# Kernel optimization log

Hardware: AMD Instinct MI355X
Metric: run time of the kernel (lower is better)

Reference implementation:

```python
import jax, jax.numpy as jnp
import numpy as np

B, T, C, H, W = 16, 8, 2048, 16, 8
C8, C4, HW, NP = C // 8, C // 4, H * W, T // 2


def _cbr(x, w, s, b):
    # 1x1 conv + folded BN (eval-mode affine) + ReLU; x: (N, Cin, H, W), w: (Cout, Cin)
    y = jnp.einsum('oc,nchw->nohw', w, x)
    return jax.nn.relu(y * s[None, :, None, None] + b[None, :, None, None])


def setup_inputs():
    key = jax.random.key(0)
    ks = jax.random.split(key, 16)
    r = lambda i, shape, sc: jax.random.normal(ks[i], shape, jnp.float32) * sc
    return dict(
        featmap=r(0, (B, T, C, H, W), 1.0),
        re_featmap=r(1, (B * T, C, H, W), 1.0),
        vect_featmap=r(2, (B, T, C), 1.0),
        embed_feat=r(3, (B, T, 128, H, W), 1.0),
        gamma_w=r(4, (C8, C), 0.03), gamma_s=jnp.ones((C8,)), gamma_b=jnp.zeros((C8,)),
        beta_w=r(5, (C8, C), 0.03), beta_s=jnp.ones((C8,)), beta_b=jnp.zeros((C8,)),
        gg_w=r(6, (128, 2 * HW), 0.05), gg_s=jnp.ones((128,)), gg_b=jnp.zeros((128,)),
        tte_w=r(7, (128, 256), 0.05), tte_s=jnp.ones((128,)), tte_b=jnp.zeros((128,)),
        te_w=r(8, (1, 256), 0.05), te_s=jnp.ones((1,)), te_b=jnp.zeros((1,)),
        theta_w=r(9, (C8, C), 0.03), theta_b=jnp.zeros((C8,)),
        cp_w1=r(10, (C8, C4), 0.05), cp_b1=jnp.zeros((C8,)),
        cp_w2=r(11, (C, C8), 0.05), cp_b2=jnp.zeros((C,)),
    )


def reference(featmap, re_featmap, vect_featmap, embed_feat,
              gamma_w, gamma_s, gamma_b, beta_w, beta_s, beta_b,
              gg_w, gg_s, gg_b, tte_w, tte_s, tte_b, te_w, te_s, te_b,
              theta_w, theta_b, cp_w1, cp_b1, cp_w2, cp_b2):
    # spatial attention embeddings: (B, T, C8, HW)
    gamma = _cbr(re_featmap, gamma_w, gamma_s, gamma_b).reshape(B, T, C8, HW)
    beta = _cbr(re_featmap, beta_w, beta_s, beta_b).reshape(B, T, C8, HW)

    # channel attention: Conv1d over time of (B, C, T) -> (B, C8, T)
    cp = jax.nn.relu(jnp.einsum('oc,btc->bot', theta_w, vect_featmap) + theta_b[None, :, None])
    cp = cp.reshape(B, C8, NP, 2)
    c0 = cp[..., 0].transpose(0, 2, 1)  # (B, NP, C8)
    c1 = cp[..., 1].transpose(0, 2, 1)

    def mlp(x):  # (B, NP, C4) -> sigmoid gate (B, NP, C)
        h1 = jax.nn.relu(x @ cp_w1.T + cp_b1)
        return jax.nn.sigmoid(h1 @ cp_w2.T + cp_b2)

    p00 = mlp(jnp.concatenate([c0, c1], -1))  # (B, NP, C)
    p01 = mlp(jnp.concatenate([c1, c0], -1))

    # pairwise spatial graphs
    g0, g1 = gamma[:, 0::2], gamma[:, 1::2]  # (B, NP, C8, HW)
    b0, b1 = beta[:, 0::2], beta[:, 1::2]
    Gs0 = jnp.einsum('bpcs,bpct->bpst', g0, b1)  # (B, NP, HW, HW)
    Gs1 = jnp.einsum('bpcs,bpct->bpst', g1, b0)
    # Gs_in = Gs^T viewed as (HW, H, W); Gs_out = Gs viewed likewise
    j0 = jnp.concatenate([Gs0.transpose(0, 1, 3, 2), Gs1], 2).reshape(B * NP, 2 * HW, H, W)
    j1 = jnp.concatenate([Gs1.transpose(0, 1, 3, 2), Gs0], 2).reshape(B * NP, 2 * HW, H, W)
    gj0 = _cbr(j0, gg_w, gg_s, gg_b)  # (B*NP, 128, H, W)
    gj1 = _cbr(j1, gg_w, gg_s, gg_b)

    ef = embed_feat.reshape(B, NP, 2, 128, H, W)
    e0 = ef[:, :, 0].reshape(B * NP, 128, H, W)
    e1 = ef[:, :, 1].reshape(B * NP, 128, H, W)
    ta = _cbr(jnp.concatenate([e0, e1], 1), tte_w, tte_s, tte_b)  # (B*NP, 128, H, W)
    tb = _cbr(jnp.concatenate([e1, e0], 1), tte_w, tte_s, tte_b)

    def gate(t_feat, gj):  # conv 256->1 + BN + sigmoid
        y = jnp.einsum('oc,nchw->nohw', te_w, jnp.concatenate([t_feat, gj], 1))
        return jax.nn.sigmoid(y * te_s[None, :, None, None] + te_b[None, :, None, None])

    pa = gate(ta, gj0).reshape(B, NP, 1, H, W)
    pb = gate(tb, gj1).reshape(B, NP, 1, H, W)

    f = featmap.reshape(B, NP, 2, C, H, W)
    gate0 = p00[..., None, None] * pa  # (B, NP, C, H, W)
    gate1 = p01[..., None, None] * pb
    out = jax.nn.relu(gate0 * f[:, :, 0] + gate1 * f[:, :, 1])
    return out * out  # (B, T//2, C, H, W)
```

## Files before the change

kernel.cpp:

```cpp
#include <hip/hip_runtime.h>
#include <stdint.h>


typedef _Float16 f16;
typedef _Float16 f16x4 __attribute__((ext_vector_type(4)));
typedef _Float16 f16x8 __attribute__((ext_vector_type(8)));
typedef float f32x4 __attribute__((ext_vector_type(4)));

typedef const void __attribute__((address_space(1)))* gptr1;
typedef void __attribute__((address_space(3)))* lptr3;

__device__ __forceinline__ void gload16(const void* g, void* l) {
  __builtin_amdgcn_global_load_lds((gptr1)g, (lptr3)l, 16, 0, 0);
}

__device__ __forceinline__ float sigmoidf_(float x) { return 1.f / (1.f + expf(-x)); }

#define WAIT_VM6 asm volatile("s_waitcnt vmcnt(6)" ::: "memory")
#define WAIT_VM0 asm volatile("s_waitcnt vmcnt(0)" ::: "memory")
#define WAIT_LGKM8 asm volatile("s_waitcnt lgkmcnt(8)" ::: "memory")
#define WAIT_LGKM0 asm volatile("s_waitcnt lgkmcnt(0)" ::: "memory")

__global__ __launch_bounds__(256) void kPP(const float* __restrict__ x,
                                           f16* __restrict__ Af,
                                           const float* __restrict__ gw, const float* __restrict__ gs,
                                           const float* __restrict__ bw, const float* __restrict__ bs,
                                           const float* __restrict__ gg_w, const float* __restrict__ gg_s,
                                           const float* __restrict__ tte_w, const float* __restrict__ tte_s,
                                           const float* __restrict__ thw, const float* __restrict__ w1,
                                           const float* __restrict__ w2,
                                           f16* __restrict__ Wf,
                                           float* __restrict__ ggT, float* __restrict__ tteT,
                                           float* __restrict__ thwT, float* __restrict__ w1T,
                                           float* __restrict__ w2T) {
  __shared__ __align__(16) char shmem[64 * 65 * 4];
  int t = threadIdx.x;
  int bid = blockIdx.x;
  if (bid < 8192) {
    float (*L)[65] = (float(*)[65])shmem;
    int n = bid >> 6;
    int kc = (bid >> 1) & 31;
    int hh = bid & 1;
    int k0 = kc * 64;
    const float* src = x + (size_t)n * 262144 + (size_t)k0 * 128 + hh * 64;
    for (int r = 0; r < 4; ++r) {
      int f = r * 256 + t;
      int kk = f >> 4, c4 = (f & 15) * 4;
      float4 v = *(const float4*)(src + (size_t)kk * 128 + c4);
      L[kk][c4 + 0] = v.x; L[kk][c4 + 1] = v.y; L[kk][c4 + 2] = v.z; L[kk][c4 + 3] = v.w;
    }
    __syncthreads();
    for (int r = 0; r < 2; ++r) {
      int id = r * 256 + t;
      int hw = id >> 3, c = id & 7;
      int cs = c ^ (hw & 7);
      f16x8 h8;
      for (int j = 0; j < 8; ++j)
        h8[j] = (f16)L[cs * 8 + j][hw];
      size_t m = (size_t)n * 128 + hh * 64 + hw;
      size_t ob = m * 2048 + (size_t)k0 + (size_t)c * 8;
      *(f16x8*)(Af + ob) = h8;
    }
    return;
  }
  if (bid < 8704) {
    int id = (bid - 8192) * 256 + t;
    int o = id >> 8, cch = id & 255;
    float s; const float* row;
    if (o < 256) { s = gs[o]; row = gw + (size_t)o * 2048; }
    else         { s = bs[o - 256]; row = bw + (size_t)(o - 256) * 2048; }
    int kb = cch >> 3, sub = cch & 7;
    int subd = sub ^ (o & 7);
    f16x8 h8;
    for (int j = 0; j < 8; ++j)
      h8[j] = (f16)(row[cch * 8 + j] * s);
    size_t ob = (size_t)o * 2048 + (size_t)kb * 64 + (size_t)subd * 8;
    *(f16x8*)(Wf + ob) = h8;
    return;
  }
  float (*TL)[65] = (float(*)[65])shmem;
  int tb = bid - 8704;
  const float* src; float* dst; const float* scale = nullptr; int R, C;
  if (tb < 128)      { src = thw;   dst = thwT; R = 256;  C = 2048; }
  else if (tb < 256) { tb -= 128; src = w2;  dst = w2T;  R = 2048; C = 256; }
  else if (tb < 288) { tb -= 256; src = w1;  dst = w1T;  R = 256;  C = 512; }
  else if (tb < 296) { tb -= 288; src = gg_w;  dst = ggT;  scale = gg_s;  R = 128; C = 256; }
  else               { tb -= 296; src = tte_w; dst = tteT; scale = tte_s; R = 128; C = 256; }
  int tpc = C >> 6;
  int r0 = (tb / tpc) * 64, c0 = (tb % tpc) * 64;
  int i16 = t >> 4, j4 = (t & 15) * 4;
  for (int s = 0; s < 4; ++s) {
    int i = i16 + s * 16;
    float4 v = *(const float4*)(src + (size_t)(r0 + i) * C + c0 + j4);
    TL[i][j4 + 0] = v.x; TL[i][j4 + 1] = v.y; TL[i][j4 + 2] = v.z; TL[i][j4 + 3] = v.w;
  }
  __syncthreads();
  for (int s = 0; s < 4; ++s) {
    int j = i16 + s * 16;
    float4 w;
    w.x = TL[j4 + 0][j]; w.y = TL[j4 + 1][j]; w.z = TL[j4 + 2][j]; w.w = TL[j4 + 3][j];
    if (scale) {
      w.x *= scale[r0 + j4 + 0]; w.y *= scale[r0 + j4 + 1];
      w.z *= scale[r0 + j4 + 2]; w.w *= scale[r0 + j4 + 3];
    }
    *(float4*)(dst + (size_t)(c0 + j) * R + r0 + j4) = w;
  }
}

__global__ __launch_bounds__(512, 2) void kGemm8(const f16* __restrict__ Af, const f16* __restrict__ Wf,
                                                 const float* __restrict__ gamma_b, const float* __restrict__ beta_b,
                                                 f16* __restrict__ gammaFh, f16* __restrict__ betaFh) {
  __shared__ __align__(16) f16 S[3][24576];
  int t = threadIdx.x;
  int lane = t & 63, wid = t >> 6;
  int wr = wid >> 2, wc = wid & 3;
  int bid = blockIdx.x;
  int bx = (bid & 7) * 16 + (bid >> 4);
  int by = (bid >> 3) & 1;
  size_t M0 = (size_t)bx * 128;
  size_t N0 = (size_t)by * 256;
  int row8 = wid * 8 + (lane >> 3);
  int sl = lane & 7;
  int fr = lane & 15, fq = lane >> 4;
  f32x4 acc[4][4] = {};
  f16x8 a[8], b[8];

  const char* AB = (const char*)Af;
  const char* WB = (const char*)Wf;
  const size_t aoff0 = (M0 + row8) * 4096 + (size_t)sl * 16;
  const size_t aoff1 = (M0 + 64 + row8) * 4096 + (size_t)sl * 16;
  const size_t woff0 = (N0 + row8) * 4096 + (size_t)sl * 16;
  const size_t woff1 = (N0 + 64 + row8) * 4096 + (size_t)sl * 16;
  const size_t woff2 = (N0 + 128 + row8) * 4096 + (size_t)sl * 16;
  const size_t woff3 = (N0 + 192 + row8) * 4096 + (size_t)sl * 16;

#define STAGE_ALL(dst, s) do {                                                     \
    int koff_ = (s) << 7;                                                          \
    char* l_ = (char*)(dst) + wid * 1024;                                          \
    gload16(AB + aoff0 + koff_, l_);                                               \
    gload16(AB + aoff1 + koff_, l_ + 8192);                                        \
    gload16(WB + woff0 + koff_, l_ + 16384);                                       \
    gload16(WB + woff1 + koff_, l_ + 24576);                                       \
    gload16(WB + woff2 + koff_, l_ + 32768);                                       \
    gload16(WB + woff3 + koff_, l_ + 40960);                                       \
  } while (0)

#define LOADG(buf, g) do {                                                         \
    const f16* bA_ = (const f16*)(buf);                                            \
    const f16* bB_ = bA_ + 8192;                                                   \
    int cg_ = (g) * 4 + fq;                                                        \
    _Pragma("unroll") for (int mi = 0; mi < 4; ++mi) {                             \
      int m_ = wr * 64 + mi * 16 + fr;                                             \
      a[(g) * 4 + mi] = *(const f16x8*)(bA_ + m_ * 64 + ((cg_ ^ (m_ & 7)) << 3));  \
    }                                                                              \
    _Pragma("unroll") for (int ni = 0; ni < 4; ++ni) {                             \
      int n_ = wc * 64 + ni * 16 + fr;                                             \
      b[(g) * 4 + ni] = *(const f16x8*)(bB_ + n_ * 64 + ((cg_ ^ (n_ & 7)) << 3));  \
    }                                                                              \
  } while (0)

#define STEP(rdbuf, stbuf, kt) do {                                                \
    if ((kt) < 31) { WAIT_VM6; } else { WAIT_VM0; }                                \
    __builtin_amdgcn_s_barrier();                                                  \
    if ((kt) <= 29) STAGE_ALL(stbuf, (kt) + 2);                                    \
    LOADG(rdbuf, 0);                                                               \
    __builtin_amdgcn_sched_barrier(0);                                             \
    LOADG(rdbuf, 1);                                                               \
    WAIT_LGKM8;                                                                    \
    __builtin_amdgcn_sched_barrier(0);                                             \
    __builtin_amdgcn_s_setprio(1);                                                 \
    _Pragma("unroll") for (int mi = 0; mi < 4; ++mi)                               \
      _Pragma("unroll") for (int ni = 0; ni < 4; ++ni)                             \
        acc[mi][ni] = __builtin_amdgcn_mfma_f32_16x16x32_f16(a[mi], b[ni], acc[mi][ni], 0, 0, 0); \
    WAIT_LGKM0;                                                                    \
    __builtin_amdgcn_sched_barrier(0);                                             \
    _Pragma("unroll") for (int mi = 0; mi < 4; ++mi)                               \
      _Pragma("unroll") for (int ni = 0; ni < 4; ++ni)                             \
        acc[mi][ni] = __builtin_amdgcn_mfma_f32_16x16x32_f16(a[4 + mi], b[4 + ni], acc[mi][ni], 0, 0, 0); \
    __builtin_amdgcn_s_setprio(0);                                                 \
  } while (0)

  STAGE_ALL(&S[0][0], 0);
  STAGE_ALL(&S[1][0], 1);
  for (int base = 0; base < 30; base += 3) {
    STEP(&S[0][0], &S[2][0], base);
    STEP(&S[1][0], &S[0][0], base + 1);
    STEP(&S[2][0], &S[1][0], base + 2);
  }
  STEP(&S[0][0], &S[2][0], 30);
  STEP(&S[1][0], &S[0][0], 31);
#undef STEP
#undef LOADG
#undef STAGE_ALL

  const float* bias = by ? beta_b : gamma_b;
  f16* outb = by ? betaFh : gammaFh;
#pragma unroll
  for (int mi = 0; mi < 4; ++mi) {
    int hwb = wr * 64 + mi * 16 + fq * 4;
#pragma unroll
    for (int ni = 0; ni < 4; ++ni) {
      int o = wc * 64 + ni * 16 + fr;
      float bb = bias[o];
      f32x4 v = acc[mi][ni];
      f16x4 w;
      w[0] = (f16)fmaxf(v[0] + bb, 0.f);
      w[1] = (f16)fmaxf(v[1] + bb, 0.f);
      w[2] = (f16)fmaxf(v[2] + bb, 0.f);
      w[3] = (f16)fmaxf(v[3] + bb, 0.f);
      *(f16x4*)(outb + (size_t)bx * 32768 + (size_t)o * 128 + hwb) = w;
    }
  }
}

__global__ __launch_bounds__(256) void kTT(const float* __restrict__ vect, const float* __restrict__ thwT,
                                           float* __restrict__ P,
                                           const float* __restrict__ embed, const float* __restrict__ tteT,
                                           const float* __restrict__ tte_b, const float* __restrict__ te_w,
                                           float* __restrict__ Sta) {
  __shared__ float V[512];
  __shared__ __align__(16) float E[256 * 64];
  __shared__ float Red2[2][16 * 64];
  int bid = blockIdx.x;
  int t = threadIdx.x;
  if (bid < 512) {
    int bt = bid & 127, kq = bid >> 7;
    const float* src = vect + (size_t)bt * 2048 + kq * 512;
    if (t < 128) *(float4*)(V + t * 4) = *(const float4*)(src + t * 4);
    __syncthreads();
    const float* wp = thwT + (size_t)kq * 512 * 256 + t;
    float acc = 0.f;
#pragma unroll 8
    for (int c = 0; c < 512; ++c)
      acc = fmaf(wp[(size_t)c * 256], V[c], acc);
    P[((size_t)kq * 128 + bt) * 256 + t] = acc;
    return;
  }
  int i = bid - 512;
  int n = i & 63, hh = (i >> 6) & 1;
  int b = n >> 2, p = n & 3;
  const float* eA = embed + (size_t)(b * 8 + 2 * p) * 16384 + hh * 64;
  const float* eB = embed + (size_t)(b * 8 + 2 * p + 1) * 16384 + hh * 64;
  for (int r = 0; r < 8; ++r) {
    int f = r * 256 + t;
    int ch = f >> 4, q = (f & 15) * 4;
    *(float4*)(E + ch * 64 + q) = *(const float4*)(eA + (size_t)ch * 128 + q);
  }
  for (int r = 0; r < 8; ++r) {
    int f = r * 256 + t;
    int ch = f >> 4, q = (f & 15) * 4;
    *(float4*)(E + (128 + ch) * 64 + q) = *(const float4*)(eB + (size_t)ch * 128 + q);
  }
  __syncthreads();
  int ty = t >> 4, tx = t & 15;
  float acc0[8][4] = {}, acc1[8][4] = {};
  for (int c = 0; c < 256; ++c) {
    float w8a[8], w8b[8];
    *(float4*)w8a = *(const float4*)(tteT + (size_t)c * 128 + ty * 8);
    *(float4*)(w8a + 4) = *(const float4*)(tteT + (size_t)c * 128 + ty * 8 + 4);
    int c2 = c ^ 128;
    *(float4*)w8b = *(const float4*)(tteT + (size_t)c2 * 128 + ty * 8);
    *(float4*)(w8b + 4) = *(const float4*)(tteT + (size_t)c2 * 128 + ty * 8 + 4);
    float4 g = *(const float4*)(E + c * 64 + tx * 4);
    for (int ii = 0; ii < 8; ++ii) {
      acc0[ii][0] = fmaf(w8a[ii], g.x, acc0[ii][0]);
      acc0[ii][1] = fmaf(w8a[ii], g.y, acc0[ii][1]);
      acc0[ii][2] = fmaf(w8a[ii], g.z, acc0[ii][2]);
      acc0[ii][3] = fmaf(w8a[ii], g.w, acc0[ii][3]);
      acc1[ii][0] = fmaf(w8b[ii], g.x, acc1[ii][0]);
      acc1[ii][1] = fmaf(w8b[ii], g.y, acc1[ii][1]);
      acc1[ii][2] = fmaf(w8b[ii], g.z, acc1[ii][2]);
      acc1[ii][3] = fmaf(w8b[ii], g.w, acc1[ii][3]);
    }
  }
  float par0[4] = {0.f, 0.f, 0.f, 0.f};
  float par1[4] = {0.f, 0.f, 0.f, 0.f};
  for (int ii = 0; ii < 8; ++ii) {
    int o = ty * 8 + ii;
    float tb = tte_b[o], tw = te_w[o];
    for (int j = 0; j < 4; ++j) {
      par0[j] += tw * fmaxf(acc0[ii][j] + tb, 0.f);
      par1[j] += tw * fmaxf(acc1[ii][j] + tb, 0.f);
    }
  }
  for (int j = 0; j < 4; ++j) {
    Red2[0][ty * 64 + tx * 4 + j] = par0[j];
    Red2[1][ty * 64 + tx * 4 + j] = par1[j];
  }
  __syncthreads();
  if (t < 128) {
    int g = t >> 6, tt = t & 63;
    float s = 0.f;
    for (int q = 0; q < 16; ++q) s += Red2[g][q * 64 + tt];
    Sta[(size_t)g * 8192 + n * 128 + hh * 64 + tt] = s;
  }
}

__global__ __launch_bounds__(256) void kAG(const float* __restrict__ P, const float* __restrict__ thb,
                                           const float* __restrict__ w1T, const float* __restrict__ b1,
                                           float* __restrict__ h1,
                                           const f16* __restrict__ gammaFh, const f16* __restrict__ betaFh,
                                           float* __restrict__ Gs0, float* __restrict__ Gs1) {
  __shared__ float x0[256], x1[256];
  __shared__ float ra[256], rb[256];
  __shared__ __align__(16) float As[16 * 128];
  __shared__ __align__(16) float Bs[16 * 64];
  int bid = blockIdx.x;
  int t = threadIdx.x;
  if (bid < 256) {
    int bp = bid & 63, och = bid >> 6;
    int b = bp >> 2, p = bp & 3;
    int bt0 = b * 8 + 2 * p, bt1 = bt0 + 1;
    {
      float a0 = 0.f, a1 = 0.f;
      for (int q = 0; q < 4; ++q) {
        a0 += P[((size_t)q * 128 + bt0) * 256 + t];
        a1 += P[((size_t)q * 128 + bt1) * 256 + t];
      }
      float tb = thb[t];
      x0[t] = fmaxf(a0 + tb, 0.f);
      x1[t] = fmaxf(a1 + tb, 0.f);
    }
    __syncthreads();
    int o = och * 64 + (t & 63);
    int ks = t >> 6;
    const float* xa = (ks < 2) ? x0 : x1;
    const float* xb = (ks < 2) ? x1 : x0;
    int kbase = ks * 128;
    int xoff = (ks < 2) ? kbase : kbase - 256;
    float aa = 0.f, ab = 0.f;
#pragma unroll 8
    for (int ii = 0; ii < 128; ++ii) {
      float w = w1T[(size_t)(kbase + ii) * 256 + o];
      aa = fmaf(w, xa[xoff + ii], aa);
      ab = fmaf(w, xb[xoff + ii], ab);
    }
    ra[t] = aa;
    rb[t] = ab;
    __syncthreads();
    if (t < 64) {
      float sa = ra[t] + ra[64 + t] + ra[128 + t] + ra[192 + t];
      float sb = rb[t] + rb[64 + t] + rb[128 + t] + rb[192 + t];
      float bb = b1[o];
      h1[((size_t)bp * 2) * 256 + o] = fmaxf(sa + bb, 0.f);
      h1[((size_t)bp * 2 + 1) * 256 + o] = fmaxf(sb + bb, 0.f);
    }
    return;
  }
  int i = bid - 256;
  int n = i & 63, which = (i >> 6) & 1, th = (i >> 7) & 1;
  int b = n >> 2, p = n & 3;
  int tg = 2 * p + which;
  int tb = 2 * p + 1 - which;
  const f16* A = gammaFh + (size_t)(b * 8 + tg) * 32768;
  const f16* Bm = betaFh + (size_t)(b * 8 + tb) * 32768;
  float* out = (which ? Gs1 : Gs0) + (size_t)n * 16384;
  int ty = t >> 4, tx = t & 15;
  float acc[8][4] = {};
  for (int c0 = 0; c0 < 256; c0 += 16) {
    {
      int cc = t >> 4, col8 = (t & 15) * 8;
      f16x8 v = *(const f16x8*)(A + (size_t)(c0 + cc) * 128 + col8);
      for (int j = 0; j < 8; ++j) As[cc * 128 + col8 + j] = (float)v[j];
    }
    if (t < 128) {
      int cc = t >> 3, col8 = (t & 7) * 8;
      f16x8 v = *(const f16x8*)(Bm + (size_t)(c0 + cc) * 128 + th * 64 + col8);
      for (int j = 0; j < 8; ++j) Bs[cc * 64 + col8 + j] = (float)v[j];
    }
    __syncthreads();
    for (int cc = 0; cc < 16; ++cc) {
      float a8[8];
      *(float4*)a8 = *(const float4*)(As + cc * 128 + ty * 8);
      *(float4*)(a8 + 4) = *(const float4*)(As + cc * 128 + ty * 8 + 4);
      float4 b4 = *(const float4*)(Bs + cc * 64 + tx * 4);
      for (int ii = 0; ii < 8; ++ii) {
        acc[ii][0] = fmaf(a8[ii], b4.x, acc[ii][0]);
        acc[ii][1] = fmaf(a8[ii], b4.y, acc[ii][1]);
        acc[ii][2] = fmaf(a8[ii], b4.z, acc[ii][2]);
        acc[ii][3] = fmaf(a8[ii], b4.w, acc[ii][3]);
      }
    }
    __syncthreads();
  }
  for (int ii = 0; ii < 8; ++ii) {
    *(float4*)(out + (size_t)(ty * 8 + ii) * 128 + th * 64 + tx * 4) =
        make_float4(acc[ii][0], acc[ii][1], acc[ii][2], acc[ii][3]);
  }
}

__global__ __launch_bounds__(256) void kBG(const float* __restrict__ h1, const float* __restrict__ w2T,
                                           const float* __restrict__ b2,
                                           float* __restrict__ p00, float* __restrict__ p01,
                                           const float* __restrict__ Gs0, const float* __restrict__ Gs1,
                                           const float* __restrict__ ggT, const float* __restrict__ gg_b,
                                           const float* __restrict__ te_w, float* __restrict__ Sgj) {
  __shared__ float ha[256], hb[256];
  __shared__ float G0h[64 * 129];
  __shared__ __align__(16) float G1c[128 * 64];
  __shared__ float Red[16 * 64];
  int bid = blockIdx.x;
  int t = threadIdx.x;
  if (bid < 512) {
    int bp = bid & 63, chc = bid >> 6;
    ha[t] = h1[((size_t)bp * 2) * 256 + t];
    hb[t] = h1[((size_t)bp * 2 + 1) * 256 + t];
    __syncthreads();
    int ch = chc * 256 + t;
    float sa = 0.f, sb = 0.f;
#pragma unroll 8
    for (int k = 0; k < 256; ++k) {
      float w = w2T[(size_t)k * 2048 + ch];
      sa = fmaf(w, ha[k], sa);
      sb = fmaf(w, hb[k], sb);
    }
    p00[(size_t)bp * 2048 + ch] = sigmoidf_(sa + b2[ch]);
    p01[(size_t)bp * 2048 + ch] = sigmoidf_(sb + b2[ch]);
    return;
  }
  int i = bid - 512;
  int n = i & 63, gate = (i >> 6) & 1, hh = (i >> 7) & 1;
  const float* srcT = (gate == 0 ? Gs0 : Gs1) + (size_t)n * 16384;
  const float* srcC = (gate == 0 ? Gs1 : Gs0) + (size_t)n * 16384;
  for (int r = 0; r < 8; ++r) {
    int f = r * 256 + t;
    int hwl = f >> 5, c4 = (f & 31) * 4;
    float4 v = *(const float4*)(srcT + (size_t)(hh * 64 + hwl) * 128 + c4);
    G0h[hwl * 129 + c4 + 0] = v.x;
    G0h[hwl * 129 + c4 + 1] = v.y;
    G0h[hwl * 129 + c4 + 2] = v.z;
    G0h[hwl * 129 + c4 + 3] = v.w;
  }
  for (int r = 0; r < 8; ++r) {
    int f = r * 256 + t;
    int c = f >> 4, q = (f & 15) * 4;
    *(float4*)(G1c + c * 64 + q) = *(const float4*)(srcC + (size_t)c * 128 + hh * 64 + q);
  }
  __syncthreads();
  int ty = t >> 4, tx = t & 15;
  float acc[8][4] = {};
  for (int c = 0; c < 128; ++c) {
    float w8[8];
    *(float4*)w8 = *(const float4*)(ggT + (size_t)c * 128 + ty * 8);
    *(float4*)(w8 + 4) = *(const float4*)(ggT + (size_t)c * 128 + ty * 8 + 4);
    float g4[4];
    for (int j = 0; j < 4; ++j) g4[j] = G0h[(tx * 4 + j) * 129 + c];
    for (int ii = 0; ii < 8; ++ii)
      for (int j = 0; j < 4; ++j)
        acc[ii][j] = fmaf(w8[ii], g4[j], acc[ii][j]);
  }
  for (int c = 0; c < 128; ++c) {
    float w8[8];
    *(float4*)w8 = *(const float4*)(ggT + (size_t)(128 + c) * 128 + ty * 8);
    *(float4*)(w8 + 4) = *(const float4*)(ggT + (size_t)(128 + c) * 128 + ty * 8 + 4);
    float4 g = *(const float4*)(G1c + c * 64 + tx * 4);
    for (int ii = 0; ii < 8; ++ii) {
      acc[ii][0] = fmaf(w8[ii], g.x, acc[ii][0]);
      acc[ii][1] = fmaf(w8[ii], g.y, acc[ii][1]);
      acc[ii][2] = fmaf(w8[ii], g.z, acc[ii][2]);
      acc[ii][3] = fmaf(w8[ii], g.w, acc[ii][3]);
    }
  }
  float par[4] = {0.f, 0.f, 0.f, 0.f};
  for (int ii = 0; ii < 8; ++ii) {
    int o = ty * 8 + ii;
    float gb = gg_b[o], tw = te_w[128 + o];
    for (int j = 0; j < 4; ++j)
      par[j] += tw * fmaxf(acc[ii][j] + gb, 0.f);
  }
  for (int j = 0; j < 4; ++j) Red[ty * 64 + tx * 4 + j] = par[j];
  __syncthreads();
  if (t < 64) {
    float s = 0.f;
    for (int g = 0; g < 16; ++g) s += Red[g * 64 + t];
    Sgj[(size_t)gate * 8192 + n * 128 + hh * 64 + t] = s;
  }
}

__global__ __launch_bounds__(256) void kFinal(const float* __restrict__ featmap, const float* __restrict__ p00,
                                              const float* __restrict__ p01, const float* __restrict__ Sta,
                                              const float* __restrict__ Sgj, const float* __restrict__ te_s,
                                              const float* __restrict__ te_b, float* __restrict__ out) {
  int fid = blockIdx.x * 256 + threadIdx.x;
  int h4 = (fid & 31) * 4;
  int c = (fid >> 5) & 2047;
  int bp = fid >> 16;
  int b = bp >> 2, p = bp & 3;
  float ga = p00[(size_t)bp * 2048 + c];
  float gb = p01[(size_t)bp * 2048 + c];
  float ts = te_s[0], tbv = te_b[0];
  float4 sa0 = *(const float4*)(Sta + (size_t)bp * 128 + h4);
  float4 sg0 = *(const float4*)(Sgj + (size_t)bp * 128 + h4);
  float4 sa1 = *(const float4*)(Sta + 8192 + (size_t)bp * 128 + h4);
  float4 sg1 = *(const float4*)(Sgj + 8192 + (size_t)bp * 128 + h4);
  float4 pa4, pb4;
  pa4.x = sigmoidf_(ts * (sa0.x + sg0.x) + tbv);
  pa4.y = sigmoidf_(ts * (sa0.y + sg0.y) + tbv);
  pa4.z = sigmoidf_(ts * (sa0.z + sg0.z) + tbv);
  pa4.w = sigmoidf_(ts * (sa0.w + sg0.w) + tbv);
  pb4.x = sigmoidf_(ts * (sa1.x + sg1.x) + tbv);
  pb4.y = sigmoidf_(ts * (sa1.y + sg1.y) + tbv);
  pb4.z = sigmoidf_(ts * (sa1.z + sg1.z) + tbv);
  pb4.w = sigmoidf_(ts * (sa1.w + sg1.w) + tbv);
  const float* f0 = featmap + (size_t)(b * 8 + 2 * p) * 262144 + (size_t)c * 128 + h4;
  const float* f1 = f0 + 262144;
  float4 v0 = *(const float4*)f0;
  float4 v1 = *(const float4*)f1;
  float4 o4;
  float r;
  r = fmaxf(ga * pa4.x * v0.x + gb * pb4.x * v1.x, 0.f); o4.x = r * r;
  r = fmaxf(ga * pa4.y * v0.y + gb * pb4.y * v1.y, 0.f); o4.y = r * r;
  r = fmaxf(ga * pa4.z * v0.z + gb * pb4.z * v1.z, 0.f); o4.z = r * r;
  r = fmaxf(ga * pa4.w * v0.w + gb * pb4.w * v1.w, 0.f); o4.w = r * r;
  *(float4*)(out + (size_t)fid * 4) = o4;
}

extern "C" void kernel_launch(void* const* d_in, const int* in_sizes, int n_in,
                              void* d_out, int out_size, void* d_ws, size_t ws_size,
                              hipStream_t stream) {
  (void)in_sizes; (void)n_in; (void)out_size; (void)ws_size;
  const float* featmap    = (const float*)d_in[0];
  const float* re_featmap = (const float*)d_in[1];
  const float* vect       = (const float*)d_in[2];
  const float* embed      = (const float*)d_in[3];
  const float* gamma_w    = (const float*)d_in[4];
  const float* gamma_s    = (const float*)d_in[5];
  const float* gamma_b    = (const float*)d_in[6];
  const float* beta_w     = (const float*)d_in[7];
  const float* beta_s     = (const float*)d_in[8];
  const float* beta_b     = (const float*)d_in[9];
  const float* gg_w       = (const float*)d_in[10];
  const float* gg_s       = (const float*)d_in[11];
  const float* gg_b       = (const float*)d_in[12];
  const float* tte_w      = (const float*)d_in[13];
  const float* tte_s      = (const float*)d_in[14];
  const float* tte_b      = (const float*)d_in[15];
  const float* te_w       = (const float*)d_in[16];
  const float* te_s       = (const float*)d_in[17];
  const float* te_b       = (const float*)d_in[18];
  const float* theta_w    = (const float*)d_in[19];
  const float* theta_b    = (const float*)d_in[20];
  const float* cp_w1      = (const float*)d_in[21];
  const float* cp_b1      = (const float*)d_in[22];
  const float* cp_w2      = (const float*)d_in[23];
  const float* cp_b2      = (const float*)d_in[24];
  float* out = (float*)d_out;

  char* w = (char*)d_ws;
  f16* Af  = (f16*)w;   w += (size_t)16384 * 2048 * 2;
  f16* Wf  = (f16*)w;   w += (size_t)512 * 2048 * 2;
  f16* gammaFh = (f16*)w; w += (size_t)128 * 256 * 128 * 2;
  f16* betaFh  = (f16*)w; w += (size_t)128 * 256 * 128 * 2;
  float* Gs0    = (float*)w; w += (size_t)64 * 128 * 128 * 4;
  float* Gs1    = (float*)w; w += (size_t)64 * 128 * 128 * 4;
  float* ggT    = (float*)w; w += (size_t)256 * 128 * 4;
  float* tteT   = (float*)w; w += (size_t)256 * 128 * 4;
  float* thwT   = (float*)w; w += (size_t)2048 * 256 * 4;
  float* w1T    = (float*)w; w += (size_t)512 * 256 * 4;
  float* w2T    = (float*)w; w += (size_t)256 * 2048 * 4;
  float* P      = (float*)w; w += (size_t)4 * 128 * 256 * 4;
  float* h1     = (float*)w; w += (size_t)64 * 2 * 256 * 4;
  float* Sta    = (float*)w; w += (size_t)2 * 64 * 128 * 4;
  float* Sgj    = (float*)w; w += (size_t)2 * 64 * 128 * 4;
  float* p00    = (float*)w; w += (size_t)64 * 2048 * 4;
  float* p01    = (float*)w; w += (size_t)64 * 2048 * 4;

  kPP<<<9008, 256, 0, stream>>>(re_featmap, Af,
                                gamma_w, gamma_s, beta_w, beta_s, gg_w, gg_s, tte_w, tte_s,
                                theta_w, cp_w1, cp_w2, Wf, ggT, tteT, thwT, w1T, w2T);
  kGemm8<<<256, 512, 0, stream>>>(Af, Wf, gamma_b, beta_b, gammaFh, betaFh);
  kTT<<<640, 256, 0, stream>>>(vect, thwT, P, embed, tteT, tte_b, te_w, Sta);
  kAG<<<512, 256, 0, stream>>>(P, theta_b, w1T, cp_b1, h1, gammaFh, betaFh, Gs0, Gs1);
  kBG<<<768, 256, 0, stream>>>(h1, w2T, cp_b2, p00, p01, Gs0, Gs1, ggT, gg_b, te_w, Sgj);
  kFinal<<<16384, 256, 0, stream>>>(featmap, p00, p01, Sta, Sgj, te_s, te_b, out);
}
```

Baseline: 269.5 us.

## Merge mid-stage kernels into two launches and shrink shared memory

Merges the three middle kernels (kTT, kAG, kBG) into two. The gamma·beta GEMM moves into the first launch next to the theta projection and the tte embedding. The whole channel MLP (theta reduce, fc1, fc2, sigmoid) now runs in one block per batch-pair, so the h1 intermediate buffer is gone. The tte path is re-tiled to 32-column halves, which doubles its block count and cuts its shared memory. The gg path reads one operand straight from global memory instead of staging it in LDS. This removes one launch and a global round-trip and should raise occupancy through smaller LDS arenas. The cost is that the MLP now runs on only 64 serial-heavy blocks, each doing 512+2048-channel dot loops.

```diff
diff --git a/kernel.cpp b/kernel.cpp
--- a/kernel.cpp
+++ b/kernel.cpp
@@ -213,17 +213,18 @@
   }
 }
 
-__global__ __launch_bounds__(256) void kTT(const float* __restrict__ vect, const float* __restrict__ thwT,
+__global__ __launch_bounds__(256) void kM1(const float* __restrict__ vect, const float* __restrict__ thwT,
                                            float* __restrict__ P,
                                            const float* __restrict__ embed, const float* __restrict__ tteT,
                                            const float* __restrict__ tte_b, const float* __restrict__ te_w,
-                                           float* __restrict__ Sta) {
-  __shared__ float V[512];
-  __shared__ __align__(16) float E[256 * 64];
-  __shared__ float Red2[2][16 * 64];
+                                           float* __restrict__ Sta,
+                                           const f16* __restrict__ gammaFh, const f16* __restrict__ betaFh,
+                                           float* __restrict__ Gs0, float* __restrict__ Gs1) {
+  __shared__ __align__(16) char arena[36992];
   int bid = blockIdx.x;
   int t = threadIdx.x;
   if (bid < 512) {
+    float* V = (float*)arena;
     int bt = bid & 127, kq = bid >> 7;
     const float* src = vect + (size_t)bt * 2048 + kq * 512;
     if (t < 128) *(float4*)(V + t * 4) = *(const float4*)(src + t * 4);
@@ -236,118 +237,67 @@
     P[((size_t)kq * 128 + bt) * 256 + t] = acc;
     return;
   }
-  int i = bid - 512;
-  int n = i & 63, hh = (i >> 6) & 1;
-  int b = n >> 2, p = n & 3;
-  const float* eA = embed + (size_t)(b * 8 + 2 * p) * 16384 + hh * 64;
-  const float* eB = embed + (size_t)(b * 8 + 2 * p + 1) * 16384 + hh * 64;
-  for (int r = 0; r < 8; ++r) {
-    int f = r * 256 + t;
-    int ch = f >> 4, q = (f & 15) * 4;
-    *(float4*)(E + ch * 64 + q) = *(const float4*)(eA + (size_t)ch * 128 + q);
-  }
-  for (int r = 0; r < 8; ++r) {
-    int f = r * 256 + t;
-    int ch = f >> 4, q = (f & 15) * 4;
-    *(float4*)(E + (128 + ch) * 64 + q) = *(const float4*)(eB + (size_t)ch * 128 + q);
-  }
-  __syncthreads();
-  int ty = t >> 4, tx = t & 15;
-  float acc0[8][4] = {}, acc1[8][4] = {};
-  for (int c = 0; c < 256; ++c) {
-    float w8a[8], w8b[8];
-    *(float4*)w8a = *(const float4*)(tteT + (size_t)c * 128 + ty * 8);
-    *(float4*)(w8a + 4) = *(const float4*)(tteT + (size_t)c * 128 + ty * 8 + 4);
-    int c2 = c ^ 128;
-    *(float4*)w8b = *(const float4*)(tteT + (size_t)c2 * 128 + ty * 8);
-    *(float4*)(w8b + 4) = *(const float4*)(tteT + (size_t)c2 * 128 + ty * 8 + 4);
-    float4 g = *(const float4*)(E + c * 64 + tx * 4);
+  if (bid < 768) {
+    float* E = (float*)arena;
+    float* Red2 = (float*)(arena + 32768);
+    int i = bid - 512;
+    int n = i & 63, hq = i >> 6;
+    int b = n >> 2, p = n & 3;
+    const float* eA = embed + (size_t)(b * 8 + 2 * p) * 16384 + hq * 32;
+    const float* eB = eA + 16384;
+    for (int r = 0; r < 4; ++r) {
+      int f = r * 256 + t;
+      int ch = f >> 3, q = (f & 7) * 4;
+      *(float4*)(E + ch * 32 + q) = *(const float4*)(eA + (size_t)ch * 128 + q);
+    }
+    for (int r = 0; r < 4; ++r) {
+      int f = r * 256 + t;
+      int ch = f >> 3, q = (f & 7) * 4;
+      *(float4*)(E + (128 + ch) * 32 + q) = *(const float4*)(eB + (size_t)ch * 128 + q);
+    }
+    __syncthreads();
+    int ty = t >> 4, tx = t & 15;
+    float acc0[8][2] = {}, acc1[8][2] = {};
+    for (int c = 0; c < 256; ++c) {
+      float w8a[8], w8b[8];
+      *(float4*)w8a = *(const float4*)(tteT + (size_t)c * 128 + ty * 8);
+      *(float4*)(w8a + 4) = *(const float4*)(tteT + (size_t)c * 128 + ty * 8 + 4);
+      int c2 = c ^ 128;
+      *(float4*)w8b = *(const float4*)(tteT + (size_t)c2 * 128 + ty * 8);
+      *(float4*)(w8b + 4) = *(const float4*)(tteT + (size_t)c2 * 128 + ty * 8 + 4);
+      float2 g = *(const float2*)(E + c * 32 + tx * 2);
+      for (int ii = 0; ii < 8; ++ii) {
+        acc0[ii][0] = fmaf(w8a[ii], g.x, acc0[ii][0]);
+        acc0[ii][1] = fmaf(w8a[ii], g.y, acc0[ii][1]);
+        acc1[ii][0] = fmaf(w8b[ii], g.x, acc1[ii][0]);
+        acc1[ii][1] = fmaf(w8b[ii], g.y, acc1[ii][1]);
+      }
+    }
+    float par0[2] = {0.f, 0.f}, par1[2] = {0.f, 0.f};
     for (int ii = 0; ii < 8; ++ii) {
-      acc0[ii][0] = fmaf(w8a[ii], g.x, acc0[ii][0]);
-      acc0[ii][1] = fmaf(w8a[ii], g.y, acc0[ii][1]);
-      acc0[ii][2] = fmaf(w8a[ii], g.z, acc0[ii][2]);
-      acc0[ii][3] = fmaf(w8a[ii], g.w, acc0[ii][3]);
-      acc1[ii][0] = fmaf(w8b[ii], g.x, acc1[ii][0]);
-      acc1[ii][1] = fmaf(w8b[ii], g.y, acc1[ii][1]);
-      acc1[ii][2] = fmaf(w8b[ii], g.z, acc1[ii][2]);
-      acc1[ii][3] = fmaf(w8b[ii], g.w, acc1[ii][3]);
-    }
-  }
-  float par0[4] = {0.f, 0.f, 0.f, 0.f};
-  float par1[4] = {0.f, 0.f, 0.f, 0.f};
-  for (int ii = 0; ii < 8; ++ii) {
-    int o = ty * 8 + ii;
-    float tb = tte_b[o], tw = te_w[o];
-    for (int j = 0; j < 4; ++j) {
-      par0[j] += tw * fmaxf(acc0[ii][j] + tb, 0.f);
-      par1[j] += tw * fmaxf(acc1[ii][j] + tb, 0.f);
-    }
-  }
-  for (int j = 0; j < 4; ++j) {
-    Red2[0][ty * 64 + tx * 4 + j] = par0[j];
-    Red2[1][ty * 64 + tx * 4 + j] = par1[j];
-  }
-  __syncthreads();
-  if (t < 128) {
-    int g = t >> 6, tt = t & 63;
-    float s = 0.f;
-    for (int q = 0; q < 16; ++q) s += Red2[g][q * 64 + tt];
-    Sta[(size_t)g * 8192 + n * 128 + hh * 64 + tt] = s;
-  }
-}
-
-__global__ __launch_bounds__(256) void kAG(const float* __restrict__ P, const float* __restrict__ thb,
-                                           const float* __restrict__ w1T, const float* __restrict__ b1,
-                                           float* __restrict__ h1,
-                                           const f16* __restrict__ gammaFh, const f16* __restrict__ betaFh,
-                                           float* __restrict__ Gs0, float* __restrict__ Gs1) {
-  __shared__ float x0[256], x1[256];
-  __shared__ float ra[256], rb[256];
-  __shared__ __align__(16) float As[16 * 128];
-  __shared__ __align__(16) float Bs[16 * 64];
-  int bid = blockIdx.x;
-  int t = threadIdx.x;
-  if (bid < 256) {
-    int bp = bid & 63, och = bid >> 6;
-    int b = bp >> 2, p = bp & 3;
-    int bt0 = b * 8 + 2 * p, bt1 = bt0 + 1;
-    {
-      float a0 = 0.f, a1 = 0.f;
-      for (int q = 0; q < 4; ++q) {
-        a0 += P[((size_t)q * 128 + bt0) * 256 + t];
-        a1 += P[((size_t)q * 128 + bt1) * 256 + t];
+      int o = ty * 8 + ii;
+      float tb = tte_b[o], tw = te_w[o];
+      for (int j = 0; j < 2; ++j) {
+        par0[j] += tw * fmaxf(acc0[ii][j] + tb, 0.f);
+        par1[j] += tw * fmaxf(acc1[ii][j] + tb, 0.f);
       }
-      float tb = thb[t];
-      x0[t] = fmaxf(a0 + tb, 0.f);
-      x1[t] = fmaxf(a1 + tb, 0.f);
-    }
-    __syncthreads();
-    int o = och * 64 + (t & 63);
-    int ks = t >> 6;
-    const float* xa = (ks < 2) ? x0 : x1;
-    const float* xb = (ks < 2) ? x1 : x0;
-    int kbase = ks * 128;
-    int xoff = (ks < 2) ? kbase : kbase - 256;
-    float aa = 0.f, ab = 0.f;
-#pragma unroll 8
-    for (int ii = 0; ii < 128; ++ii) {
-      float w = w1T[(size_t)(kbase + ii) * 256 + o];
-      aa = fmaf(w, xa[xoff + ii], aa);
-      ab = fmaf(w, xb[xoff + ii], ab);
-    }
-    ra[t] = aa;
-    rb[t] = ab;
+    }
+    for (int j = 0; j < 2; ++j) {
+      Red2[0 * 512 + ty * 32 + tx * 2 + j] = par0[j];
+      Red2[1 * 512 + ty * 32 + tx * 2 + j] = par1[j];
+    }
     __syncthreads();
     if (t < 64) {
-      float sa = ra[t] + ra[64 + t] + ra[128 + t] + ra[192 + t];
-      float sb = rb[t] + rb[64 + t] + rb[128 + t] + rb[192 + t];
-      float bb = b1[o];
-      h1[((size_t)bp * 2) * 256 + o] = fmaxf(sa + bb, 0.f);
-      h1[((size_t)bp * 2 + 1) * 256 + o] = fmaxf(sb + bb, 0.f);
+      int g = t >> 5, tt = t & 31;
+      float s = 0.f;
+      for (int q = 0; q < 16; ++q) s += Red2[g * 512 + q * 32 + tt];
+      Sta[(size_t)g * 8192 + n * 128 + hq * 32 + tt] = s;
     }
     return;
   }
-  int i = bid - 256;
+  float* As = (float*)arena;
+  float* Bs = (float*)(arena + 8192);
+  int i = bid - 768;
   int n = i & 63, which = (i >> 6) & 1, th = (i >> 7) & 1;
   int b = n >> 2, p = n & 3;
   int tg = 2 * p + which;
@@ -389,91 +339,121 @@
   }
 }
 
-__global__ __launch_bounds__(256) void kBG(const float* __restrict__ h1, const float* __restrict__ w2T,
-                                           const float* __restrict__ b2,
-                                           float* __restrict__ p00, float* __restrict__ p01,
-                                           const float* __restrict__ Gs0, const float* __restrict__ Gs1,
+__global__ __launch_bounds__(256) void kM2(const float* __restrict__ Gs0, const float* __restrict__ Gs1,
                                            const float* __restrict__ ggT, const float* __restrict__ gg_b,
-                                           const float* __restrict__ te_w, float* __restrict__ Sgj) {
-  __shared__ float ha[256], hb[256];
-  __shared__ float G0h[64 * 129];
-  __shared__ __align__(16) float G1c[128 * 64];
-  __shared__ float Red[16 * 64];
+                                           const float* __restrict__ te_w, float* __restrict__ Sgj,
+                                           const float* __restrict__ P, const float* __restrict__ thb,
+                                           const float* __restrict__ w1T, const float* __restrict__ b1,
+                                           const float* __restrict__ w2T, const float* __restrict__ b2,
+                                           float* __restrict__ p00, float* __restrict__ p01) {
+  __shared__ __align__(16) char arena[37248];
   int bid = blockIdx.x;
   int t = threadIdx.x;
-  if (bid < 512) {
-    int bp = bid & 63, chc = bid >> 6;
-    ha[t] = h1[((size_t)bp * 2) * 256 + t];
-    hb[t] = h1[((size_t)bp * 2 + 1) * 256 + t];
-    __syncthreads();
-    int ch = chc * 256 + t;
+  if (bid < 256) {
+    float* G0h = (float*)arena;
+    float* Red = (float*)(arena + 33024);
+    int n = bid & 63, gate = (bid >> 6) & 1, hh = (bid >> 7) & 1;
+    const float* srcT = (gate == 0 ? Gs0 : Gs1) + (size_t)n * 16384;
+    const float* srcC = (gate == 0 ? Gs1 : Gs0) + (size_t)n * 16384 + hh * 64;
+    for (int r = 0; r < 8; ++r) {
+      int f = r * 256 + t;
+      int hwl = f >> 5, c4 = (f & 31) * 4;
+      float4 v = *(const float4*)(srcT + (size_t)(hh * 64 + hwl) * 128 + c4);
+      G0h[hwl * 129 + c4 + 0] = v.x;
+      G0h[hwl * 129 + c4 + 1] = v.y;
+      G0h[hwl * 129 + c4 + 2] = v.z;
+      G0h[hwl * 129 + c4 + 3] = v.w;
+    }
+    __syncthreads();
+    int ty = t >> 4, tx = t & 15;
+    float acc[8][4] = {};
+    for (int c = 0; c < 128; ++c) {
+      float w8[8];
+      *(float4*)w8 = *(const float4*)(ggT + (size_t)c * 128 + ty * 8);
+      *(float4*)(w8 + 4) = *(const float4*)(ggT + (size_t)c * 128 + ty * 8 + 4);
+      float g4[4];
+      for (int j = 0; j < 4; ++j) g4[j] = G0h[(tx * 4 + j) * 129 + c];
+      for (int ii = 0; ii < 8; ++ii)
+        for (int j = 0; j < 4; ++j)
+          acc[ii][j] = fmaf(w8[ii], g4[j], acc[ii][j]);
+    }
+    for (int c = 0; c < 128; ++c) {
+      float w8[8];
+      *(float4*)w8 = *(const float4*)(ggT + (size_t)(128 + c) * 128 + ty * 8);
+      *(float4*)(w8 + 4) = *(const float4*)(ggT + (size_t)(128 + c) * 128 + ty * 8 + 4);
+      float4 g = *(const float4*)(srcC + (size_t)c * 128 + tx * 4);
+      for (int ii = 0; ii < 8; ++ii) {
+        acc[ii][0] = fmaf(w8[ii], g.x, acc[ii][0]);
+        acc[ii][1] = fmaf(w8[ii], g.y, acc[ii][1]);
+        acc[ii][2] = fmaf(w8[ii], g.z, acc[ii][2]);
+        acc[ii][3] = fmaf(w8[ii], g.w, acc[ii][3]);
+      }
+    }
+    float par[4] = {0.f, 0.f, 0.f, 0.f};
+    for (int ii = 0; ii < 8; ++ii) {
+      int o = ty * 8 + ii;
+      float gb = gg_b[o], tw = te_w[128 + o];
+      for (int j = 0; j < 4; ++j)
+        par[j] += tw * fmaxf(acc[ii][j] + gb, 0.f);
+    }
+    for (int j = 0; j < 4; ++j) Red[ty * 64 + tx * 4 + j] = par[j];
+    __syncthreads();
+    if (t < 64) {
+      float s = 0.f;
+      for (int g = 0; g < 16; ++g) s += Red[g * 64 + t];
+      Sgj[(size_t)gate * 8192 + n * 128 + hh * 64 + t] = s;
+    }
+    return;
+  }
+  float* x0 = (float*)arena;
+  float* x1 = x0 + 256;
+  float* h1a = x0 + 512;
+  float* h1b = x0 + 768;
+  int bp = bid - 256;
+  int b = bp >> 2, p = bp & 3;
+  int bt0 = b * 8 + 2 * p, bt1 = bt0 + 1;
+  {
+    float a0 = 0.f, a1 = 0.f;
+    for (int q = 0; q < 4; ++q) {
+      a0 += P[((size_t)q * 128 + bt0) * 256 + t];
+      a1 += P[((size_t)q * 128 + bt1) * 256 + t];
+    }
+    float tb = thb[t];
+    x0[t] = fmaxf(a0 + tb, 0.f);
+    x1[t] = fmaxf(a1 + tb, 0.f);
+  }
+  __syncthreads();
+  {
+    float aa = 0.f, ab = 0.f;
+    const float* wp = w1T + t;
+#pragma unroll 4
+    for (int k = 0; k < 256; ++k) {
+      float w = wp[(size_t)k * 256];
+      aa = fmaf(w, x0[k], aa);
+      ab = fmaf(w, x1[k], ab);
+    }
+#pragma unroll 4
+    for (int k = 0; k < 256; ++k) {
+      float w = wp[(size_t)(256 + k) * 256];
+      aa = fmaf(w, x1[k], aa);
+      ab = fmaf(w, x0[k], ab);
+    }
+    float bb = b1[t];
+    h1a[t] = fmaxf(aa + bb, 0.f);
+    h1b[t] = fmaxf(ab + bb, 0.f);
+  }
+  __syncthreads();
+  for (int r = 0; r < 8; ++r) {
+    int ch = r * 256 + t;
     float sa = 0.f, sb = 0.f;
-#pragma unroll 8
+#pragma unroll 4
     for (int k = 0; k < 256; ++k) {
       float w = w2T[(size_t)k * 2048 + ch];
-      sa = fmaf(w, ha[k], sa);
-      sb = fmaf(w, hb[k], sb);
+      sa = fmaf(w, h1a[k], sa);
+      sb = fmaf(w, h1b[k], sb);
     }
     p00[(size_t)bp * 2048 + ch] = sigmoidf_(sa + b2[ch]);
     p01[(size_t)bp * 2048 + ch] = sigmoidf_(sb + b2[ch]);
-    return;
-  }
-  int i = bid - 512;
-  int n = i & 63, gate = (i >> 6) & 1, hh = (i >> 7) & 1;
-  const float* srcT = (gate == 0 ? Gs0 : Gs1) + (size_t)n * 16384;
-  const float* srcC = (gate == 0 ? Gs1 : Gs0) + (size_t)n * 16384;
-  for (int r = 0; r < 8; ++r) {
-    int f = r * 256 + t;
-    int hwl = f >> 5, c4 = (f & 31) * 4;
-    float4 v = *(const float4*)(srcT + (size_t)(hh * 64 + hwl) * 128 + c4);
-    G0h[hwl * 129 + c4 + 0] = v.x;
-    G0h[hwl * 129 + c4 + 1] = v.y;
-    G0h[hwl * 129 + c4 + 2] = v.z;
-    G0h[hwl * 129 + c4 + 3] = v.w;
-  }
-  for (int r = 0; r < 8; ++r) {
-    int f = r * 256 + t;
-    int c = f >> 4, q = (f & 15) * 4;
-    *(float4*)(G1c + c * 64 + q) = *(const float4*)(srcC + (size_t)c * 128 + hh * 64 + q);
-  }
-  __syncthreads();
-  int ty = t >> 4, tx = t & 15;
-  float acc[8][4] = {};
-  for (int c = 0; c < 128; ++c) {
-    float w8[8];
-    *(float4*)w8 = *(const float4*)(ggT + (size_t)c * 128 + ty * 8);
-    *(float4*)(w8 + 4) = *(const float4*)(ggT + (size_t)c * 128 + ty * 8 + 4);
-    float g4[4];
-    for (int j = 0; j < 4; ++j) g4[j] = G0h[(tx * 4 + j) * 129 + c];
-    for (int ii = 0; ii < 8; ++ii)
-      for (int j = 0; j < 4; ++j)
-        acc[ii][j] = fmaf(w8[ii], g4[j], acc[ii][j]);
-  }
-  for (int c = 0; c < 128; ++c) {
-    float w8[8];
-    *(float4*)w8 = *(const float4*)(ggT + (size_t)(128 + c) * 128 + ty * 8);
-    *(float4*)(w8 + 4) = *(const float4*)(ggT + (size_t)(128 + c) * 128 + ty * 8 + 4);
-    float4 g = *(const float4*)(G1c + c * 64 + tx * 4);
-    for (int ii = 0; ii < 8; ++ii) {
-      acc[ii][0] = fmaf(w8[ii], g.x, acc[ii][0]);
-      acc[ii][1] = fmaf(w8[ii], g.y, acc[ii][1]);
-      acc[ii][2] = fmaf(w8[ii], g.z, acc[ii][2]);
-      acc[ii][3] = fmaf(w8[ii], g.w, acc[ii][3]);
-    }
-  }
-  float par[4] = {0.f, 0.f, 0.f, 0.f};
-  for (int ii = 0; ii < 8; ++ii) {
-    int o = ty * 8 + ii;
-    float gb = gg_b[o], tw = te_w[128 + o];
-    for (int j = 0; j < 4; ++j)
-      par[j] += tw * fmaxf(acc[ii][j] + gb, 0.f);
-  }
-  for (int j = 0; j < 4; ++j) Red[ty * 64 + tx * 4 + j] = par[j];
-  __syncthreads();
-  if (t < 64) {
-    float s = 0.f;
-    for (int g = 0; g < 16; ++g) s += Red[g * 64 + t];
-    Sgj[(size_t)gate * 8192 + n * 128 + hh * 64 + t] = s;
   }
 }
 
@@ -559,7 +539,6 @@
   float* w1T    = (float*)w; w += (size_t)512 * 256 * 4;
   float* w2T    = (float*)w; w += (size_t)256 * 2048 * 4;
   float* P      = (float*)w; w += (size_t)4 * 128 * 256 * 4;
-  float* h1     = (float*)w; w += (size_t)64 * 2 * 256 * 4;
   float* Sta    = (float*)w; w += (size_t)2 * 64 * 128 * 4;
   float* Sgj    = (float*)w; w += (size_t)2 * 64 * 128 * 4;
   float* p00    = (float*)w; w += (size_t)64 * 2048 * 4;
@@ -569,8 +548,9 @@
                                 gamma_w, gamma_s, beta_w, beta_s, gg_w, gg_s, tte_w, tte_s,
                                 theta_w, cp_w1, cp_w2, Wf, ggT, tteT, thwT, w1T, w2T);
   kGemm8<<<256, 512, 0, stream>>>(Af, Wf, gamma_b, beta_b, gammaFh, betaFh);
-  kTT<<<640, 256, 0, stream>>>(vect, thwT, P, embed, tteT, tte_b, te_w, Sta);
-  kAG<<<512, 256, 0, stream>>>(P, theta_b, w1T, cp_b1, h1, gammaFh, betaFh, Gs0, Gs1);
-  kBG<<<768, 256, 0, stream>>>(h1, w2T, cp_b2, p00, p01, Gs0, Gs1, ggT, gg_b, te_w, Sgj);
+  kM1<<<1024, 256, 0, stream>>>(vect, thwT, P, embed, tteT, tte_b, te_w, Sta,
+                                gammaFh, betaFh, Gs0, Gs1);
+  kM2<<<320, 256, 0, stream>>>(Gs0, Gs1, ggT, gg_b, te_w, Sgj,
+                               P, theta_b, w1T, cp_b1, w2T, cp_b2, p00, p01);
   kFinal<<<16384, 256, 0, stream>>>(featmap, p00, p01, Sta, Sgj, te_s, te_b, out);
 }
```

Result: slower. 393.4 us (+46.0%).
